# Kernel optimization log

Hardware: AMD Instinct MI355X
Metric: run time of the kernel (lower is better)

Reference implementation:

```python
import jax, jax.numpy as jnp
import numpy as np

B, S = 16, 8192
D_MODEL = 128          # config.moe_intermediate_size
D_HID = 512            # config.intermediate_size
N_EXPERTS = 8
BEH_DIM = 32           # config.behavior_embedding_dim
N_BEH = 16             # config.num_behavior -> embedding rows = N_BEH + 1


def setup_inputs() -> dict:
    key = jax.random.key(0)
    k1, k2, k3, k4, k5, k6 = jax.random.split(key, 6)
    hidden_states = jax.random.normal(k1, (B, S, D_MODEL), dtype=jnp.float32)
    position_index = jax.random.randint(k2, (B, S), 0, N_EXPERTS, dtype=jnp.int32)
    behavior_index = jax.random.randint(k3, (B, S), 0, N_BEH + 1, dtype=jnp.int32)
    din = D_MODEL + BEH_DIM
    # expert weights: wi maps (D_MODEL+BEH_DIM)->D_HID, wo maps D_HID->D_MODEL (no bias)
    Wi = jax.random.normal(k4, (N_EXPERTS, din, D_HID), dtype=jnp.float32) * (din ** -0.5)
    Wo = jax.random.normal(k5, (N_EXPERTS, D_HID, D_MODEL), dtype=jnp.float32) * (D_HID ** -0.5)
    emb = jax.random.normal(k6, (N_BEH + 1, BEH_DIM), dtype=jnp.float32)
    return {"hidden_states": hidden_states, "position_index": position_index,
            "behavior_index": behavior_index, "Wi": Wi, "Wo": Wo, "emb": emb}


def reference(hidden_states, position_index, behavior_index, Wi, Wo, emb):
    # behavior injection: concat learned behavior embedding onto each token
    x = jnp.concatenate([hidden_states, emb[behavior_index]], axis=-1)  # [B,S,Din]
    out = jnp.zeros_like(hidden_states)
    # sparse expert dispatch: each token routed to exactly one expert by position_index
    # (loop over small fixed expert count; dropout is identity at p=0 / eval)
    for e in range(Wi.shape[0]):
        h = jax.nn.relu(jnp.einsum('bsd,dh->bsh', x, Wi[e]))   # [B,S,H]
        y = jnp.einsum('bsh,hd->bsd', h, Wo[e])                # [B,S,D]
        out = out + jnp.where((position_index == e)[..., None], y, 0.0)
    return out
```

## Files before the change

kernel.cpp:

```cpp
#include <hip/hip_runtime.h>
#include <stdint.h>

typedef short bf16x8 __attribute__((ext_vector_type(8)));
typedef float f32x4 __attribute__((ext_vector_type(4)));
typedef unsigned short ushort_t;
typedef ushort_t ushort8 __attribute__((ext_vector_type(8)));

#define TOKENS 131072
#define DMODEL 128
#define DIN 160
#define DHID 512
#define NEXP 8
#define BEH 32
#define CAP 24576
#define MT 64
#define TILES (CAP / MT)

#define OFF_COUNTS 0
#define OFF_LISTS  1024
#define OFF_WIP    (OFF_LISTS + NEXP*CAP*4)
#define OFF_WOP    (OFF_WIP + 8*32*5*64*8*2)

#define SCATTER_BLOCKS (TOKENS / 256)
#define NWI (8*32*5*64)
#define NWO (8*8*16*64)
#define PACK_BLOCKS ((NWI + NWO + 255) / 256)

#define STEP_SHORTS 9216

typedef const __attribute__((address_space(1))) uint32_t* gu32p;
typedef __attribute__((address_space(3))) uint32_t* lu32p;

__device__ __forceinline__ ushort_t f2b(float f) {
    union { float f; uint32_t u; } x; x.f = f;
    uint32_t r = x.u + 0x7FFF + ((x.u >> 16) & 1);
    return (ushort_t)(r >> 16);
}

__device__ __forceinline__ uint32_t pk2(float lo, float hi) {
    uint32_t a = __float_as_uint(lo) + 0x8000u;
    uint32_t b = __float_as_uint(hi) + 0x8000u;
    return (a >> 16) | (b & 0xFFFF0000u);
}

__global__ __launch_bounds__(256) void prep_kernel(
    const int* __restrict__ pos, int* __restrict__ counts, int* __restrict__ lists,
    const float* __restrict__ Wi, const float* __restrict__ Wo,
    ushort_t* __restrict__ wiP, ushort_t* __restrict__ woP)
{
    __shared__ int lcnt[NEXP];
    __shared__ int lbase[NEXP];
    int tid = threadIdx.x;
    if (blockIdx.x < SCATTER_BLOCKS) {
        if (tid < NEXP) lcnt[tid] = 0;
        __syncthreads();
        int t = blockIdx.x * 256 + tid;
        int e = pos[t];
        int slot = atomicAdd(&lcnt[e], 1);
        __syncthreads();
        if (tid < NEXP) lbase[tid] = atomicAdd(&counts[tid], lcnt[tid]);
        __syncthreads();
        int p = lbase[e] + slot;
        if (p < CAP) lists[e * CAP + p] = t;
        return;
    }
    int idx = (blockIdx.x - SCATTER_BLOCKS) * 256 + tid;
    if (idx < NWI) {
        int L = idx & 63; int r = idx >> 6;
        int s = r % 5; r /= 5;
        int t1 = r & 31; int e = r >> 5;
        int i = L & 15;
        int u = t1 & 1, sI = t1 >> 1;
        int n = sI * 32 + (i >> 2) * 8 + u * 4 + (i & 3);
        int kb = s * 32 + ((L >> 4) & 3) * 8;
        ushort8 o;
        #pragma unroll
        for (int j = 0; j < 8; ++j)
            o[j] = f2b(Wi[((size_t)e * DIN + kb + j) * DHID + n]);
        *(ushort8*)(wiP + (size_t)idx * 8) = o;
    } else {
        int i2 = idx - NWI;
        if (i2 >= NWO) return;
        int L = i2 & 63; int r = i2 >> 6;
        int ks = r & 15; r >>= 4;
        int t2 = r & 7; int e = r >> 3;
        int n = t2 * 16 + (L & 15);
        int kb = ks * 32 + ((L >> 4) & 3) * 8;
        ushort8 o;
        #pragma unroll
        for (int j = 0; j < 8; ++j)
            o[j] = f2b(Wo[((size_t)e * DHID + kb + j) * DMODEL + n]);
        *(ushort8*)(woP + (size_t)i2 * 8) = o;
    }
}

__device__ __forceinline__ void stage_step(
    const ushort_t* __restrict__ wiPe, const ushort_t* __restrict__ woPe,
    ushort_t* dstBuf, int step, int tid)
{
    #pragma unroll
    for (int it = 0; it < 5; ++it) {
        int g = it * 256 + tid;
        if (it == 4 && tid >= 128) break;
        const ushort_t* src;
        if (g < 640) {
            src = wiPe + (size_t)step * 5120 + (size_t)g * 8;
        } else {
            int g2 = g - 640;
            src = woPe + ((size_t)(((g2 >> 6) * 16 + step) * 64 + (g2 & 63))) * 8;
        }
        __builtin_amdgcn_global_load_lds((gu32p)(const void*)src,
                                         (lu32p)(void*)(dstBuf + g * 8), 16, 0, 0);
    }
}

__device__ __forceinline__ bf16x8 load_x8(const float* __restrict__ hidden,
                                          const float* __restrict__ emb,
                                          int t, int bi, int c0) {
    if (t < 0) return (bf16x8)0;
    const float* src = (c0 < DMODEL) ? (hidden + (size_t)t * DMODEL + c0)
                                     : (emb + (size_t)bi * BEH + (c0 - DMODEL));
    f32x4 p0 = *(const f32x4*)src;
    f32x4 p1 = *(const f32x4*)(src + 4);
    uint32_t d0 = pk2(p0[0], p0[1]), d1 = pk2(p0[2], p0[3]);
    uint32_t d2 = pk2(p1[0], p1[1]), d3 = pk2(p1[2], p1[3]);
    return __builtin_bit_cast(bf16x8, (uint4){d0, d1, d2, d3});
}

__global__ __launch_bounds__(256, 4) void expert_gemm(
    const float* __restrict__ hidden, const int* __restrict__ bindex,
    const int* __restrict__ lists, const int* __restrict__ counts,
    const ushort_t* __restrict__ wiP, const ushort_t* __restrict__ woP,
    const float* __restrict__ emb, float* __restrict__ out)
{
    int e = blockIdx.y;
    int tile = blockIdx.x;
    int count = counts[e]; if (count > CAP) count = CAP;
    int base = tile * MT;
    if (base >= count) return;
    int mvalid = count - base; if (mvalid > MT) mvalid = MT;

    __shared__ ushort_t wbuf[2][STEP_SHORTS];

    int tid = threadIdx.x;
    int lane = tid & 63;
    int w = tid >> 6;
    int l15 = lane & 15;
    int quad = lane >> 4;

    const int* listE = lists + (size_t)e * CAP + base;
    const ushort_t* wiPe = wiP + (size_t)e * 32 * 5 * 64 * 8;
    const ushort_t* woPe = woP + (size_t)e * 8 * 16 * 64 * 8;

    stage_step(wiPe, woPe, wbuf[0], 0, tid);

    bf16x8 xf[5];
    int row = w * 16 + l15;
    int tok = -1, bi = 0;
    if (row < mvalid) { tok = listE[row]; bi = bindex[tok]; }
    #pragma unroll
    for (int s = 0; s < 5; ++s)
        xf[s] = load_x8(hidden, emb, tok, bi, s * 32 + quad * 8);

    f32x4 yacc[8] = {};

    #pragma unroll 2
    for (int step = 0; step < 16; ++step) {
        int cur = step & 1;
        __syncthreads();
        if (step + 1 < 16)
            stage_step(wiPe, woPe, wbuf[cur ^ 1], step + 1, tid);

        const ushort_t* wiS = wbuf[cur];
        const ushort_t* woS = wbuf[cur] + 5120;

        f32x4 hacc[2] = {};
        #pragma unroll
        for (int s = 0; s < 5; ++s) {
            bf16x8 a0 = *(const bf16x8*)&wiS[(0 * 5 + s) * 512 + lane * 8];
            bf16x8 a1 = *(const bf16x8*)&wiS[(1 * 5 + s) * 512 + lane * 8];
            hacc[0] = __builtin_amdgcn_mfma_f32_16x16x32_bf16(a0, xf[s], hacc[0], 0, 0, 0);
            hacc[1] = __builtin_amdgcn_mfma_f32_16x16x32_bf16(a1, xf[s], hacc[1], 0, 0, 0);
        }
        f32x4 h0 = hacc[0], h1 = hacc[1];
        #pragma unroll
        for (int r = 0; r < 4; ++r) {
            h0[r] = h0[r] > 0.f ? h0[r] : 0.f;
            h1[r] = h1[r] > 0.f ? h1[r] : 0.f;
        }
        uint4 dv = { pk2(h0[0], h0[1]), pk2(h0[2], h0[3]),
                     pk2(h1[0], h1[1]), pk2(h1[2], h1[3]) };
        bf16x8 afrag = __builtin_bit_cast(bf16x8, dv);

        #pragma unroll
        for (int n = 0; n < 8; ++n) {
            bf16x8 b = *(const bf16x8*)&woS[(n * 64 + lane) * 8];
            yacc[n] = __builtin_amdgcn_mfma_f32_16x16x32_bf16(afrag, b, yacc[n], 0, 0, 0);
        }
    }

    #pragma unroll
    for (int r = 0; r < 4; ++r) {
        int orow = w * 16 + quad * 4 + r;
        if (orow < mvalid) {
            int t = listE[orow];
            float* dst = out + (size_t)t * DMODEL + l15;
            #pragma unroll
            for (int n = 0; n < 8; ++n)
                dst[n * 16] = yacc[n][r];
        }
    }
}

extern "C" void kernel_launch(void* const* d_in, const int* in_sizes, int n_in,
                              void* d_out, int out_size, void* d_ws, size_t ws_size,
                              hipStream_t stream) {
    const float* hidden = (const float*)d_in[0];
    const int*   pos    = (const int*)d_in[1];
    const int*   beh    = (const int*)d_in[2];
    const float* Wi     = (const float*)d_in[3];
    const float* Wo     = (const float*)d_in[4];
    const float* emb    = (const float*)d_in[5];

    char* ws = (char*)d_ws;
    int* counts   = (int*)(ws + OFF_COUNTS);
    int* lists    = (int*)(ws + OFF_LISTS);
    ushort_t* wiP = (ushort_t*)(ws + OFF_WIP);
    ushort_t* woP = (ushort_t*)(ws + OFF_WOP);

    hipMemsetAsync(counts, 0, NEXP * sizeof(int), stream);
    prep_kernel<<<SCATTER_BLOCKS + PACK_BLOCKS, 256, 0, stream>>>(pos, counts, lists, Wi, Wo, wiP, woP);
    expert_gemm<<<dim3(TILES, NEXP), 256, 0, stream>>>(
        hidden, beh, lists, counts, wiP, woP, emb, (float*)d_out);
}
```

Before: 77.18 us.

## Switch expert GEMM to 32x32x16 MFMA with two-wave 64-token blocks

Replaces the 16x16x32 bf16 MFMA tiles with 32x32x16 MFMA, repacking Wi and Wo into new fragment layouts and changing the LDS staging pattern to match. Each block now runs 128 threads (two waves of 32 tokens each) instead of four waves of 16, so every wave reuses each staged weight fragment across more tokens. The goal is fewer LDS reads and MFMA issues per FLOP. The cost is fewer waves per block to hide staging latency, plus higher register pressure from the 16-wide accumulators and ten x fragments.

```diff
diff --git a/kernel.cpp b/kernel.cpp
--- a/kernel.cpp
+++ b/kernel.cpp
@@ -3,6 +3,7 @@
 
 typedef short bf16x8 __attribute__((ext_vector_type(8)));
 typedef float f32x4 __attribute__((ext_vector_type(4)));
+typedef float f32x16 __attribute__((ext_vector_type(16)));
 typedef unsigned short ushort_t;
 typedef ushort_t ushort8 __attribute__((ext_vector_type(8)));
 
@@ -19,11 +20,11 @@
 #define OFF_COUNTS 0
 #define OFF_LISTS  1024
 #define OFF_WIP    (OFF_LISTS + NEXP*CAP*4)
-#define OFF_WOP    (OFF_WIP + 8*32*5*64*8*2)
+#define OFF_WOP    (OFF_WIP + 8*16*10*64*8*2)
 
 #define SCATTER_BLOCKS (TOKENS / 256)
-#define NWI (8*32*5*64)
-#define NWO (8*8*16*64)
+#define NWI (8*16*10*64)
+#define NWO (8*4*32*64)
 #define PACK_BLOCKS ((NWI + NWO + 255) / 256)
 
 #define STEP_SHORTS 9216
@@ -67,29 +68,29 @@
     int idx = (blockIdx.x - SCATTER_BLOCKS) * 256 + tid;
     if (idx < NWI) {
         int L = idx & 63; int r = idx >> 6;
-        int s = r % 5; r /= 5;
-        int t1 = r & 31; int e = r >> 5;
-        int i = L & 15;
-        int u = t1 & 1, sI = t1 >> 1;
-        int n = sI * 32 + (i >> 2) * 8 + u * 4 + (i & 3);
-        int kb = s * 32 + ((L >> 4) & 3) * 8;
+        int f = r % 10; r /= 10;
+        int step = r & 15; int e = r >> 4;
+        int H = step * 32 + (L & 31);
+        int kb = f * 16 + ((L >> 5) & 1) * 8;
         ushort8 o;
         #pragma unroll
         for (int j = 0; j < 8; ++j)
-            o[j] = f2b(Wi[((size_t)e * DIN + kb + j) * DHID + n]);
+            o[j] = f2b(Wi[((size_t)e * DIN + kb + j) * DHID + H]);
         *(ushort8*)(wiP + (size_t)idx * 8) = o;
     } else {
         int i2 = idx - NWI;
         if (i2 >= NWO) return;
         int L = i2 & 63; int r = i2 >> 6;
-        int ks = r & 15; r >>= 4;
-        int t2 = r & 7; int e = r >> 3;
-        int n = t2 * 16 + (L & 15);
-        int kb = ks * 32 + ((L >> 4) & 3) * 8;
+        int sub = r & 31; r >>= 5;
+        int n = r & 3; int e = r >> 2;
+        int hb = sub * 16 + 4 * ((L >> 5) & 1);
+        int dm = n * 32 + (L & 31);
         ushort8 o;
         #pragma unroll
-        for (int j = 0; j < 8; ++j)
-            o[j] = f2b(Wo[((size_t)e * DHID + kb + j) * DMODEL + n]);
+        for (int j = 0; j < 8; ++j) {
+            int H = hb + (j & 3) + 8 * (j >> 2);
+            o[j] = f2b(Wo[((size_t)e * DHID + H) * DMODEL + dm]);
+        }
         *(ushort8*)(woP + (size_t)i2 * 8) = o;
     }
 }
@@ -99,15 +100,15 @@
     ushort_t* dstBuf, int step, int tid)
 {
     #pragma unroll
-    for (int it = 0; it < 5; ++it) {
-        int g = it * 256 + tid;
-        if (it == 4 && tid >= 128) break;
+    for (int it = 0; it < 9; ++it) {
+        int g = it * 128 + tid;
         const ushort_t* src;
         if (g < 640) {
             src = wiPe + (size_t)step * 5120 + (size_t)g * 8;
         } else {
             int g2 = g - 640;
-            src = woPe + ((size_t)(((g2 >> 6) * 16 + step) * 64 + (g2 & 63))) * 8;
+            int n = g2 >> 7;
+            src = woPe + (size_t)(n * 32 + 2 * step) * 512 + (size_t)(g2 & 127) * 8;
         }
         __builtin_amdgcn_global_load_lds((gu32p)(const void*)src,
                                          (lu32p)(void*)(dstBuf + g * 8), 16, 0, 0);
@@ -127,7 +128,7 @@
     return __builtin_bit_cast(bf16x8, (uint4){d0, d1, d2, d3});
 }
 
-__global__ __launch_bounds__(256, 4) void expert_gemm(
+__global__ __launch_bounds__(128, 2) void expert_gemm(
     const float* __restrict__ hidden, const int* __restrict__ bindex,
     const int* __restrict__ lists, const int* __restrict__ counts,
     const ushort_t* __restrict__ wiP, const ushort_t* __restrict__ woP,
@@ -145,24 +146,24 @@
     int tid = threadIdx.x;
     int lane = tid & 63;
     int w = tid >> 6;
-    int l15 = lane & 15;
-    int quad = lane >> 4;
+    int l31 = lane & 31;
+    int hi = lane >> 5;
 
     const int* listE = lists + (size_t)e * CAP + base;
-    const ushort_t* wiPe = wiP + (size_t)e * 32 * 5 * 64 * 8;
-    const ushort_t* woPe = woP + (size_t)e * 8 * 16 * 64 * 8;
+    const ushort_t* wiPe = wiP + (size_t)e * 16 * 10 * 64 * 8;
+    const ushort_t* woPe = woP + (size_t)e * 4 * 32 * 64 * 8;
 
     stage_step(wiPe, woPe, wbuf[0], 0, tid);
 
-    bf16x8 xf[5];
-    int row = w * 16 + l15;
+    bf16x8 xf[10];
+    int row = w * 32 + l31;
     int tok = -1, bi = 0;
     if (row < mvalid) { tok = listE[row]; bi = bindex[tok]; }
     #pragma unroll
-    for (int s = 0; s < 5; ++s)
-        xf[s] = load_x8(hidden, emb, tok, bi, s * 32 + quad * 8);
-
-    f32x4 yacc[8] = {};
+    for (int f = 0; f < 10; ++f)
+        xf[f] = load_x8(hidden, emb, tok, bi, f * 16 + hi * 8);
+
+    f32x16 yacc[4] = {};
 
     #pragma unroll 2
     for (int step = 0; step < 16; ++step) {
@@ -174,40 +175,42 @@
         const ushort_t* wiS = wbuf[cur];
         const ushort_t* woS = wbuf[cur] + 5120;
 
-        f32x4 hacc[2] = {};
-        #pragma unroll
-        for (int s = 0; s < 5; ++s) {
-            bf16x8 a0 = *(const bf16x8*)&wiS[(0 * 5 + s) * 512 + lane * 8];
-            bf16x8 a1 = *(const bf16x8*)&wiS[(1 * 5 + s) * 512 + lane * 8];
-            hacc[0] = __builtin_amdgcn_mfma_f32_16x16x32_bf16(a0, xf[s], hacc[0], 0, 0, 0);
-            hacc[1] = __builtin_amdgcn_mfma_f32_16x16x32_bf16(a1, xf[s], hacc[1], 0, 0, 0);
-        }
-        f32x4 h0 = hacc[0], h1 = hacc[1];
-        #pragma unroll
-        for (int r = 0; r < 4; ++r) {
-            h0[r] = h0[r] > 0.f ? h0[r] : 0.f;
-            h1[r] = h1[r] > 0.f ? h1[r] : 0.f;
-        }
-        uint4 dv = { pk2(h0[0], h0[1]), pk2(h0[2], h0[3]),
-                     pk2(h1[0], h1[1]), pk2(h1[2], h1[3]) };
-        bf16x8 afrag = __builtin_bit_cast(bf16x8, dv);
-
-        #pragma unroll
-        for (int n = 0; n < 8; ++n) {
-            bf16x8 b = *(const bf16x8*)&woS[(n * 64 + lane) * 8];
-            yacc[n] = __builtin_amdgcn_mfma_f32_16x16x32_bf16(afrag, b, yacc[n], 0, 0, 0);
+        f32x16 hacc = (f32x16)0;
+        #pragma unroll
+        for (int f = 0; f < 10; ++f) {
+            bf16x8 a = *(const bf16x8*)&wiS[f * 512 + lane * 8];
+            hacc = __builtin_amdgcn_mfma_f32_32x32x16_bf16(a, xf[f], hacc, 0, 0, 0);
+        }
+
+        #pragma unroll
+        for (int sg = 0; sg < 2; ++sg) {
+            float h[8];
+            #pragma unroll
+            for (int j = 0; j < 8; ++j) {
+                float v = hacc[sg * 8 + j];
+                h[j] = v > 0.f ? v : 0.f;
+            }
+            uint4 dv = { pk2(h[0], h[1]), pk2(h[2], h[3]),
+                         pk2(h[4], h[5]), pk2(h[6], h[7]) };
+            bf16x8 afrag = __builtin_bit_cast(bf16x8, dv);
+            #pragma unroll
+            for (int n = 0; n < 4; ++n) {
+                bf16x8 b = *(const bf16x8*)&woS[(n * 2 + sg) * 512 + lane * 8];
+                yacc[n] = __builtin_amdgcn_mfma_f32_32x32x16_bf16(afrag, b, yacc[n], 0, 0, 0);
+            }
         }
     }
 
     #pragma unroll
-    for (int r = 0; r < 4; ++r) {
-        int orow = w * 16 + quad * 4 + r;
+    for (int reg = 0; reg < 16; ++reg) {
+        int tr = (reg & 3) + 8 * (reg >> 2) + 4 * hi;
+        int orow = w * 32 + tr;
         if (orow < mvalid) {
             int t = listE[orow];
-            float* dst = out + (size_t)t * DMODEL + l15;
+            float* dst = out + (size_t)t * DMODEL + l31;
             #pragma unroll
-            for (int n = 0; n < 8; ++n)
-                dst[n * 16] = yacc[n][r];
+            for (int n = 0; n < 4; ++n)
+                dst[n * 32] = yacc[n][reg];
         }
     }
 }
@@ -230,6 +233,6 @@
 
     hipMemsetAsync(counts, 0, NEXP * sizeof(int), stream);
     prep_kernel<<<SCATTER_BLOCKS + PACK_BLOCKS, 256, 0, stream>>>(pos, counts, lists, Wi, Wo, wiP, woP);
-    expert_gemm<<<dim3(TILES, NEXP), 256, 0, stream>>>(
+    expert_gemm<<<dim3(TILES, NEXP), 128, 0, stream>>>(
         hidden, beh, lists, counts, wiP, woP, emb, (float*)d_out);
 }
```

Result: slower. 90.90 us (+17.8%).
